# Optimization experiments

Measured on AMD Instinct MI355X. Metric: run time of the kernel, lower is better.

## Reference

```python
import jax, jax.numpy as jnp
import numpy as np

N_NODES = 50000
N_EDGES = 800000
IN_CH = 128
HID = 64
HEADS = 4
OUT_CH = 64
NEG_SLOPE = 0.2


def _add_self_loops(ei, n):
    loops = jnp.tile(jnp.arange(n, dtype=ei.dtype)[None, :], (2, 1))
    return jnp.concatenate([ei, loops], axis=1)


def _gat_conv(x, ei, W, a_s, a_d, b, concat):
    """PyG-style GATConv. x:[N,F], ei:[2,E], W:[F,H*C], a_s/a_d:[H,C]."""
    N = x.shape[0]
    H, C = a_s.shape
    h = (x @ W).reshape(N, H, C)                     # [N,H,C]
    src, dst = ei[0], ei[1]
    al_s = (h * a_s[None]).sum(-1)                   # [N,H]
    al_d = (h * a_d[None]).sum(-1)                   # [N,H]
    logits = jax.nn.leaky_relu(al_s[src] + al_d[dst], NEG_SLOPE)  # [E,H]
    # segment softmax over incoming edges of each dst node
    m = jax.ops.segment_max(logits, dst, num_segments=N)
    m = jax.lax.stop_gradient(jnp.where(jnp.isfinite(m), m, 0.0))
    ex = jnp.exp(logits - m[dst])
    denom = jax.ops.segment_sum(ex, dst, num_segments=N)
    alpha = ex / (denom[dst] + 1e-16)                # [E,H]
    out = jax.ops.segment_sum(alpha[:, :, None] * h[src], dst, num_segments=N)  # [N,H,C]
    out = out.reshape(N, H * C) if concat else out.mean(axis=1)
    return out + b


def _hetero_layer(x, edges, self_loop_flags, W, a_s, a_d, b, concat):
    N = x.shape[0]
    out = None
    for r in range(3):
        ei = _add_self_loops(edges[r], N) if self_loop_flags[r] else edges[r]
        o = _gat_conv(x, ei, W[r], a_s[r], a_d[r], b[r], concat)
        out = o if out is None else out + o
    return out


def setup_inputs() -> dict:
    key = jax.random.key(0)
    ks = jax.random.split(key, 16)
    s = 0.05
    return {
        "x": jax.random.normal(ks[0], (N_NODES, IN_CH), jnp.float32),
        "e_blocks": jax.random.randint(ks[1], (2, N_EDGES), 0, N_NODES),
        "e_spatial": jax.random.randint(ks[2], (2, N_EDGES), 0, N_NODES),
        "e_similar": jax.random.randint(ks[3], (2, N_EDGES), 0, N_NODES),
        "W1": jax.random.normal(ks[4], (3, IN_CH, HEADS * HID), jnp.float32) * s,
        "a1s": jax.random.normal(ks[5], (3, HEADS, HID), jnp.float32) * s,
        "a1d": jax.random.normal(ks[6], (3, HEADS, HID), jnp.float32) * s,
        "b1": jax.random.normal(ks[7], (3, HEADS * HID), jnp.float32) * s,
        "W2": jax.random.normal(ks[8], (3, HEADS * HID, HEADS * HID), jnp.float32) * s,
        "a2s": jax.random.normal(ks[9], (3, HEADS, HID), jnp.float32) * s,
        "a2d": jax.random.normal(ks[10], (3, HEADS, HID), jnp.float32) * s,
        "b2": jax.random.normal(ks[11], (3, HID), jnp.float32) * s,
        "Wl": jax.random.normal(ks[12], (HID, OUT_CH), jnp.float32) * s,
        "bl": jax.random.normal(ks[13], (OUT_CH,), jnp.float32) * s,
    }


def reference(x, e_blocks, e_spatial, e_similar, W1, a1s, a1d, b1,
              W2, a2s, a2d, b2, Wl, bl):
    edges = [e_blocks, e_spatial, e_similar]
    self_loops = [False, True, True]  # 'blocks' has add_self_loops=False
    h = _hetero_layer(x, edges, self_loops, W1, a1s, a1d, b1, concat=True)
    h = jax.nn.relu(h)
    h = _hetero_layer(h, edges, self_loops, W2, a2s, a2d, b2, concat=False)
    h = jax.nn.relu(h)
    return h @ Wl + bl
```

## Files before the change

kernel.cpp:

```cpp
#include <hip/hip_runtime.h>
#include <hip/hip_bf16.h>
#include <hip/hip_fp16.h>

#define NN 50000
#define NE 800000
#define FIN 128
#define HCC 256
#define OC 64
#define NSL 0.2f
#define NT3 (3 * NN)

typedef __attribute__((ext_vector_type(8))) short sh8;
typedef __attribute__((ext_vector_type(8))) unsigned short u16x8;
typedef __attribute__((ext_vector_type(16))) float f32x16;

struct __attribute__((aligned(8))) h4 { __half x, y, z, w; };

__device__ __forceinline__ unsigned short bf_rne(float f) {
  unsigned u = __float_as_uint(f);
  u += 0x7FFF + ((u >> 16) & 1);
  return (unsigned short)(u >> 16);
}

__device__ __forceinline__ float hbits2f(unsigned short u) {
  __half_raw hr; hr.x = u;
  return __half2float((__half)hr);
}

__device__ __forceinline__ float edge_w(float lg) {
  lg = (lg > 0.f) ? lg : NSL * lg;
  return __expf(lg);
}

template<int KK>
__global__ __launch_bounds__(256) void k_prep(const float* __restrict__ W,
                                              short* __restrict__ out) {
  int i = blockIdx.x * 256 + threadIdx.x;
  if (i >= 3 * KK * 256) return;
  int r = i / (KK * 256);
  int rem = i - r * KK * 256;
  int k = rem >> 8;
  int n = rem & 255;
  float f = W[i];
  unsigned short hb = bf_rne(f);
  float hf = __uint_as_float(((unsigned)hb) << 16);
  unsigned short lb = bf_rne(f - hf);
  int cb = n >> 7, c = n & 127, ks8 = k >> 3, kj = k & 7;
  size_t base = (size_t)r * 4 * KK * 128;
  size_t oh = base + ((size_t)((cb * 2 + 0) * (KK / 8) + ks8) * 128 + c) * 8 + kj;
  size_t ol = base + ((size_t)((cb * 2 + 1) * (KK / 8) + ks8) * 128 + c) * 8 + kj;
  out[oh] = (short)hb;
  out[ol] = (short)lb;
}

__global__ void k_hist(const int* __restrict__ dst, int* __restrict__ deg, int n) {
  int i = blockIdx.x * blockDim.x + threadIdx.x;
  int st = gridDim.x * blockDim.x;
  for (; i < n; i += st) atomicAdd(&deg[dst[i]], 1);
}

__global__ __launch_bounds__(1024) void k_bsum(const int* __restrict__ deg3,
                                               int* __restrict__ bsum) {
  __shared__ int s[1024];
  int t = threadIdx.x;
  int i = blockIdx.x * 1024 + t;
  s[t] = (i < NT3) ? deg3[i] : 0;
  __syncthreads();
  for (int off = 512; off > 0; off >>= 1) {
    if (t < off) s[t] += s[t + off];
    __syncthreads();
  }
  if (t == 0) bsum[blockIdx.x] = s[0];
}

__global__ __launch_bounds__(256) void k_scan2(const int* __restrict__ bsum,
                                               int* __restrict__ boffs, int nb) {
  __shared__ int s[256];
  int t = threadIdx.x;
  int v = (t < nb) ? bsum[t] : 0;
  s[t] = v;
  __syncthreads();
  for (int off = 1; off < 256; off <<= 1) {
    int x = (t >= off) ? s[t - off] : 0;
    __syncthreads();
    s[t] += x;
    __syncthreads();
  }
  if (t < nb) boffs[t] = s[t] - v;
}

__global__ __launch_bounds__(1024) void k_rowptr(const int* __restrict__ deg3,
                                                 const int* __restrict__ boffs,
                                                 int* __restrict__ rpA,
                                                 int* __restrict__ cursor3) {
  __shared__ int s[1024];
  int t = threadIdx.x;
  int i = blockIdx.x * 1024 + t;
  int d = (i < NT3) ? deg3[i] : 0;
  s[t] = d;
  __syncthreads();
  for (int off = 1; off < 1024; off <<= 1) {
    int x = (t >= off) ? s[t - off] : 0;
    __syncthreads();
    s[t] += x;
    __syncthreads();
  }
  if (i < NT3) {
    int excl = boffs[blockIdx.x] + s[t] - d;
    int r = (i < NN) ? 0 : ((i < 2 * NN) ? 1 : 2);
    int n = i - r * NN;
    int val = excl - r * NE;
    rpA[r * (NN + 1) + n] = val;
    cursor3[i] = val;
  }
  if (blockIdx.x == 0 && t < 3) rpA[t * (NN + 1) + NN] = NE;
}

__global__ void k_scatter(const int* __restrict__ srcv, const int* __restrict__ dstv,
                          int* __restrict__ cursor, int* __restrict__ csr_src, int n) {
  int i = blockIdx.x * blockDim.x + threadIdx.x;
  int st = gridDim.x * blockDim.x;
  for (; i < n; i += st) {
    int pos = atomicAdd(&cursor[dstv[i]], 1);
    csr_src[pos] = srcv[i];
  }
}

template<int KK, bool AF32>
__global__ __launch_bounds__(256) void k_mgemm(const void* __restrict__ Av,
                                               const short* __restrict__ BcAll,
                                               const float* __restrict__ asfAll,
                                               const float* __restrict__ adfAll,
                                               __half* __restrict__ houtAll,
                                               float* __restrict__ alsAll,
                                               float* __restrict__ aldAll, int M) {
  const int rel = blockIdx.y;
  const short* Bc = BcAll + (size_t)rel * 4 * KK * 128;
  const float* asf = asfAll + rel * HCC;
  const float* adf = adfAll + rel * HCC;
  __half* hout = houtAll + (size_t)rel * NN * HCC;
  float* als = alsAll + (size_t)rel * NN * 4;
  float* ald = aldAll + (size_t)rel * NN * 4;

  const int tid = threadIdx.x;
  const int lane = tid & 63;
  const int w = tid >> 6;
  const int l31 = lane & 31;
  const int lg = lane >> 5;
  const int wrow = blockIdx.x * 64 + (w & 1) * 32;
  const int ch = w >> 1;

  f32x16 acc[4];
#pragma unroll
  for (int t = 0; t < 4; ++t) acc[t] = (f32x16)(0.f);

  const int r = wrow + l31;
  const bool aok = r < M;
  const float* apf = (const float*)Av + (size_t)r * KK;
  const __half* aph = (const __half*)Av + (size_t)r * KK;
  const short* bh = Bc + (size_t)(ch * 2 + 0) * KK * 128 + l31 * 8;
  const short* bl = Bc + (size_t)(ch * 2 + 1) * KK * 128 + l31 * 8;

#pragma unroll 2
  for (int kst = 0; kst < KK / 16; ++kst) {
    const int k0 = kst * 16 + lg * 8;
    float fa[8];
    if (AF32) {
      float4 x0 = make_float4(0.f, 0.f, 0.f, 0.f), x1 = x0;
      if (aok) {
        x0 = *(const float4*)(apf + k0);
        x1 = *(const float4*)(apf + k0 + 4);
      }
      fa[0] = x0.x; fa[1] = x0.y; fa[2] = x0.z; fa[3] = x0.w;
      fa[4] = x1.x; fa[5] = x1.y; fa[6] = x1.z; fa[7] = x1.w;
    } else {
      u16x8 hv = {0, 0, 0, 0, 0, 0, 0, 0};
      if (aok) hv = *(const u16x8*)(aph + k0);
#pragma unroll
      for (int j = 0; j < 8; ++j) fa[j] = hbits2f(hv[j]);
    }
    const int ks8 = kst * 2 + lg;
    const short* bhp = bh + (size_t)ks8 * 1024;
    const short* blp = bl + (size_t)ks8 * 1024;
    sh8 bhf[4], blf[4];
#pragma unroll
    for (int t = 0; t < 4; ++t) {
      bhf[t] = *(const sh8*)(bhp + t * 256);
      blf[t] = *(const sh8*)(blp + t * 256);
    }
    sh8 ahi, alo;
#pragma unroll
    for (int j = 0; j < 8; ++j) {
      float f = fa[j];
      unsigned short hb = bf_rne(f);
      float hf = __uint_as_float(((unsigned)hb) << 16);
      unsigned short lb = bf_rne(f - hf);
      ahi[j] = (short)hb;
      alo[j] = (short)lb;
    }
#pragma unroll
    for (int t = 0; t < 4; ++t) {
      acc[t] = __builtin_amdgcn_mfma_f32_32x32x16_bf16(ahi, bhf[t], acc[t], 0, 0, 0);
      acc[t] = __builtin_amdgcn_mfma_f32_32x32x16_bf16(alo, bhf[t], acc[t], 0, 0, 0);
      acc[t] = __builtin_amdgcn_mfma_f32_32x32x16_bf16(ahi, blf[t], acc[t], 0, 0, 0);
    }
  }

  float asr[4], adr[4];
#pragma unroll
  for (int t = 0; t < 4; ++t) {
    int col = ch * 128 + t * 32 + l31;
    asr[t] = asf[col];
    adr[t] = adf[col];
  }
#pragma unroll
  for (int v = 0; v < 16; ++v) {
    const int rl = (v & 3) + 8 * (v >> 2) + 4 * lg;
    const int row = wrow + rl;
    const bool rok = row < M;
    float s0 = 0.f, s1 = 0.f, d0 = 0.f, d1 = 0.f;
    __half* hp = hout + (size_t)row * 256 + ch * 128 + l31;
#pragma unroll
    for (int t = 0; t < 4; ++t) {
      float dv = acc[t][v];
      if (rok) hp[t * 32] = __float2half(dv);
      if (t < 2) { s0 += dv * asr[t]; d0 += dv * adr[t]; }
      else       { s1 += dv * asr[t]; d1 += dv * adr[t]; }
    }
#pragma unroll
    for (int m = 1; m < 32; m <<= 1) {
      s0 += __shfl_xor(s0, m);
      s1 += __shfl_xor(s1, m);
      d0 += __shfl_xor(d0, m);
      d1 += __shfl_xor(d1, m);
    }
    if (rok && l31 == 0) {
      *(float2*)(als + (size_t)row * 4 + ch * 2) = make_float2(s0, s1);
      *(float2*)(ald + (size_t)row * 4 + ch * 2) = make_float2(d0, d1);
    }
  }
}

template<bool SL>
__device__ __forceinline__ void gat_rel(int n, int head, size_t loff,
                                        const __half* __restrict__ h,
                                        const float* __restrict__ als,
                                        const float* __restrict__ ald,
                                        const int* __restrict__ rp,
                                        const int* __restrict__ cs,
                                        float& ox, float& oy, float& oz, float& ow) {
  float ad = ald[n * 4 + head];
  int rs = rp[n], re = rp[n + 1];
  float ax = 0.f, ay = 0.f, az = 0.f, aw = 0.f, wsum = 0.f;
  int i = rs;
  for (; i + 4 <= re; i += 4) {
    int s0 = cs[i], s1 = cs[i + 1], s2 = cs[i + 2], s3 = cs[i + 3];
    float al0 = als[s0 * 4 + head];
    float al1 = als[s1 * 4 + head];
    float al2 = als[s2 * 4 + head];
    float al3 = als[s3 * 4 + head];
    h4 v0 = *(const h4*)&h[(size_t)s0 * HCC + loff];
    h4 v1 = *(const h4*)&h[(size_t)s1 * HCC + loff];
    h4 v2 = *(const h4*)&h[(size_t)s2 * HCC + loff];
    h4 v3 = *(const h4*)&h[(size_t)s3 * HCC + loff];
    float w0 = edge_w(al0 + ad), w1 = edge_w(al1 + ad);
    float w2 = edge_w(al2 + ad), w3 = edge_w(al3 + ad);
    wsum += (w0 + w1) + (w2 + w3);
    ax = fmaf(w0, __half2float(v0.x), ax); ay = fmaf(w0, __half2float(v0.y), ay);
    az = fmaf(w0, __half2float(v0.z), az); aw = fmaf(w0, __half2float(v0.w), aw);
    ax = fmaf(w1, __half2float(v1.x), ax); ay = fmaf(w1, __half2float(v1.y), ay);
    az = fmaf(w1, __half2float(v1.z), az); aw = fmaf(w1, __half2float(v1.w), aw);
    ax = fmaf(w2, __half2float(v2.x), ax); ay = fmaf(w2, __half2float(v2.y), ay);
    az = fmaf(w2, __half2float(v2.z), az); aw = fmaf(w2, __half2float(v2.w), aw);
    ax = fmaf(w3, __half2float(v3.x), ax); ay = fmaf(w3, __half2float(v3.y), ay);
    az = fmaf(w3, __half2float(v3.z), az); aw = fmaf(w3, __half2float(v3.w), aw);
  }
  for (; i < re; ++i) {
    int s = cs[i];
    float w = edge_w(als[s * 4 + head] + ad);
    wsum += w;
    h4 hv = *(const h4*)&h[(size_t)s * HCC + loff];
    ax = fmaf(w, __half2float(hv.x), ax);
    ay = fmaf(w, __half2float(hv.y), ay);
    az = fmaf(w, __half2float(hv.z), az);
    aw = fmaf(w, __half2float(hv.w), aw);
  }
  if (SL) {
    float w = edge_w(als[n * 4 + head] + ad);
    wsum += w;
    h4 hv = *(const h4*)&h[(size_t)n * HCC + loff];
    ax = fmaf(w, __half2float(hv.x), ax);
    ay = fmaf(w, __half2float(hv.y), ay);
    az = fmaf(w, __half2float(hv.z), az);
    aw = fmaf(w, __half2float(hv.w), aw);
  }
  float inv = 1.0f / (wsum + 1e-16f);
  ox = fmaf(ax, inv, ox);
  oy = fmaf(ay, inv, oy);
  oz = fmaf(az, inv, oz);
  ow = fmaf(aw, inv, ow);
}

template<bool CONCAT>
__global__ __launch_bounds__(256) void k_gather3(const __half* __restrict__ h3,
                                                 const float* __restrict__ als3,
                                                 const float* __restrict__ ald3,
                                                 const int* __restrict__ rpA,
                                                 const int* __restrict__ cs0,
                                                 const int* __restrict__ cs1,
                                                 const int* __restrict__ cs2,
                                                 const float* __restrict__ bias,
                                                 __half* __restrict__ o16,
                                                 float* __restrict__ o32) {
  int gid = blockIdx.x * blockDim.x + threadIdx.x;
  int n = gid >> 6;
  int lane = threadIdx.x & 63;
  if (n >= NN) return;
  int head = lane >> 4;
  size_t loff = (size_t)lane * 4;
  const size_t HS = (size_t)NN * HCC;
  const size_t AS = (size_t)NN * 4;
  float ox = 0.f, oy = 0.f, oz = 0.f, ow = 0.f;
  gat_rel<false>(n, head, loff, h3,          als3,          ald3,          rpA,               cs0, ox, oy, oz, ow);
  gat_rel<true >(n, head, loff, h3 + HS,     als3 + AS,     ald3 + AS,     rpA + (NN + 1),    cs1, ox, oy, oz, ow);
  gat_rel<true >(n, head, loff, h3 + 2 * HS, als3 + 2 * AS, ald3 + 2 * AS, rpA + 2 * (NN + 1), cs2, ox, oy, oz, ow);
  if (CONCAT) {
    float4 b0 = *(const float4*)&bias[lane * 4];
    float4 b1 = *(const float4*)&bias[HCC + lane * 4];
    float4 b2 = *(const float4*)&bias[2 * HCC + lane * 4];
    h4 o;
    o.x = __float2half(fmaxf(ox + b0.x + b1.x + b2.x, 0.f));
    o.y = __float2half(fmaxf(oy + b0.y + b1.y + b2.y, 0.f));
    o.z = __float2half(fmaxf(oz + b0.z + b1.z + b2.z, 0.f));
    o.w = __float2half(fmaxf(ow + b0.w + b1.w + b2.w, 0.f));
    *(h4*)&o16[(size_t)n * HCC + loff] = o;
  } else {
    ox += __shfl_xor(ox, 16); oy += __shfl_xor(oy, 16);
    oz += __shfl_xor(oz, 16); ow += __shfl_xor(ow, 16);
    ox += __shfl_xor(ox, 32); oy += __shfl_xor(oy, 32);
    oz += __shfl_xor(oz, 32); ow += __shfl_xor(ow, 32);
    if (lane < 16) {
      float4 b0 = *(const float4*)&bias[lane * 4];
      float4 b1 = *(const float4*)&bias[OC + lane * 4];
      float4 b2 = *(const float4*)&bias[2 * OC + lane * 4];
      float4 o;
      o.x = 0.25f * ox + b0.x + b1.x + b2.x;
      o.y = 0.25f * oy + b0.y + b1.y + b2.y;
      o.z = 0.25f * oz + b0.z + b1.z + b2.z;
      o.w = 0.25f * ow + b0.w + b1.w + b2.w;
      *(float4*)&o32[(size_t)n * OC + lane * 4] = o;
    }
  }
}

__global__ __launch_bounds__(256) void k_final(const float* __restrict__ out2,
                                               const float* __restrict__ Wl,
                                               const float* __restrict__ bl,
                                               float* __restrict__ outp) {
  __shared__ float Ws[64 * 64];
  __shared__ float bs[64];
  int tid = threadIdx.x;
  for (int i = tid; i < 4096; i += 256) Ws[i] = Wl[i];
  if (tid < 64) bs[tid] = bl[tid];
  __syncthreads();
  int r = blockIdx.x * 4 + (tid >> 6);
  int c = tid & 63;
  if (r >= NN) return;
  const float* xr = &out2[(size_t)r * OC];
  float acc = bs[c];
#pragma unroll
  for (int k = 0; k < 64; ++k) {
    float xv = xr[k];
    xv = (xv > 0.f) ? xv : 0.f;
    acc = fmaf(xv, Ws[k * 64 + c], acc);
  }
  outp[(size_t)r * OC + c] = acc;
}

extern "C" void kernel_launch(void* const* d_in, const int* in_sizes, int n_in,
                              void* d_out, int out_size, void* d_ws, size_t ws_size,
                              hipStream_t stream) {
  const float* x   = (const float*)d_in[0];
  const int* e_b   = (const int*)d_in[1];
  const int* e_sp  = (const int*)d_in[2];
  const int* e_si  = (const int*)d_in[3];
  const float* W1  = (const float*)d_in[4];
  const float* a1s = (const float*)d_in[5];
  const float* a1d = (const float*)d_in[6];
  const float* b1  = (const float*)d_in[7];
  const float* W2  = (const float*)d_in[8];
  const float* a2s = (const float*)d_in[9];
  const float* a2d = (const float*)d_in[10];
  const float* b2  = (const float*)d_in[11];
  const float* Wl  = (const float*)d_in[12];
  const float* bl  = (const float*)d_in[13];
  float* out = (float*)d_out;

  char* ws = (char*)d_ws;
  size_t off = 0;
  auto alloc = [&](size_t b) {
    char* p = ws + off;
    off += (b + 255) & ~(size_t)255;
    return p;
  };
  __half* h3   = (__half*)alloc((size_t)3 * NN * HCC * 2);
  __half* out1h = (__half*)alloc((size_t)NN * HCC * 2);
  float* out2 = (float*)out1h;
  float* als3 = (float*)alloc((size_t)3 * NN * 4 * 4);
  float* ald3 = (float*)alloc((size_t)3 * NN * 4 * 4);
  int* deg3   = (int*)alloc((size_t)NT3 * 4);
  int* cursor3= (int*)alloc((size_t)NT3 * 4);
  int* rpA    = (int*)alloc((size_t)3 * (NN + 1) * 4);
  int* bsum   = (int*)alloc(256 * 4);
  int* boffs  = (int*)alloc(256 * 4);
  short* Wc1  = (short*)alloc((size_t)3 * 4 * FIN * 128 * 2);
  short* Wc2  = (short*)alloc((size_t)3 * 4 * HCC * 128 * 2);
  int* cs[3];
  for (int r = 0; r < 3; ++r) cs[r] = (int*)alloc((size_t)NE * 4);

  const int* edges[3] = {e_b, e_sp, e_si};

  k_prep<FIN><<<(3 * FIN * 256 + 255) / 256, 256, 0, stream>>>(W1, Wc1);
  k_prep<HCC><<<(3 * HCC * 256 + 255) / 256, 256, 0, stream>>>(W2, Wc2);

  hipMemsetAsync(deg3, 0, (size_t)NT3 * 4, stream);
  for (int r = 0; r < 3; ++r)
    k_hist<<<1024, 256, 0, stream>>>(edges[r] + NE, deg3 + r * NN, NE);
  const int NB = (NT3 + 1023) / 1024;
  k_bsum<<<NB, 1024, 0, stream>>>(deg3, bsum);
  k_scan2<<<1, 256, 0, stream>>>(bsum, boffs, NB);
  k_rowptr<<<NB, 1024, 0, stream>>>(deg3, boffs, rpA, cursor3);
  for (int r = 0; r < 3; ++r)
    k_scatter<<<1024, 256, 0, stream>>>(edges[r], edges[r] + NE, cursor3 + r * NN, cs[r], NE);

  const int gblocks = (NN + 63) / 64;
  const int ablocks = (NN * 64) / 256;

  k_mgemm<FIN, true><<<dim3(gblocks, 3), 256, 0, stream>>>(
      x, Wc1, a1s, a1d, h3, als3, ald3, NN);
  k_gather3<true><<<ablocks, 256, 0, stream>>>(
      h3, als3, ald3, rpA, cs[0], cs[1], cs[2], b1, out1h, nullptr);

  k_mgemm<HCC, false><<<dim3(gblocks, 3), 256, 0, stream>>>(
      out1h, Wc2, a2s, a2d, h3, als3, ald3, NN);
  k_gather3<false><<<ablocks, 256, 0, stream>>>(
      h3, als3, ald3, rpA, cs[0], cs[1], cs[2], b2, nullptr, out2);

  k_final<<<(NN + 3) / 4, 256, 0, stream>>>(out2, Wl, bl, out);
}
```

Baseline: 907.1 us.

## Precompute edge weights, pre-split GEMM inputs to bf16 hi/lo, merge CSR kernels

A new per-node kernel computes the exponentiated edge attention weights once, together with per-node weight sums and self-loop weights, before each aggregation pass. The gather kernel then reads these instead of recomputing exp and the softmax denominator for every one of the 64 lanes, and it now unrolls by 8. The bf16 hi/lo split of the GEMM input moves out of the GEMM inner loop: x is split by a separate kernel, and the layer-1 output is written directly as hi/lo bf16 (replacing fp16). The per-relation histogram and scatter launches are merged into single kernels. The cost is extra memory traffic for the edge weight array (3×NE×4 floats) and for the two-plane activations.

```diff
diff --git a/kernel.cpp b/kernel.cpp
--- a/kernel.cpp
+++ b/kernel.cpp
@@ -11,20 +11,15 @@
 #define NT3 (3 * NN)
 
 typedef __attribute__((ext_vector_type(8))) short sh8;
-typedef __attribute__((ext_vector_type(8))) unsigned short u16x8;
 typedef __attribute__((ext_vector_type(16))) float f32x16;
 
 struct __attribute__((aligned(8))) h4 { __half x, y, z, w; };
+struct __attribute__((aligned(8))) s4 { short x, y, z, w; };
 
 __device__ __forceinline__ unsigned short bf_rne(float f) {
   unsigned u = __float_as_uint(f);
   u += 0x7FFF + ((u >> 16) & 1);
   return (unsigned short)(u >> 16);
-}
-
-__device__ __forceinline__ float hbits2f(unsigned short u) {
-  __half_raw hr; hr.x = u;
-  return __half2float((__half)hr);
 }
 
 __device__ __forceinline__ float edge_w(float lg) {
@@ -53,10 +48,32 @@
   out[ol] = (short)lb;
 }
 
-__global__ void k_hist(const int* __restrict__ dst, int* __restrict__ deg, int n) {
+__global__ __launch_bounds__(256) void k_split(const float* __restrict__ x,
+                                               short* __restrict__ xhi,
+                                               short* __restrict__ xlo) {
+  int i = blockIdx.x * 256 + threadIdx.x;
+  if (i >= NN * FIN / 4) return;
+  float4 v = ((const float4*)x)[i];
+  s4 h, l;
+  float f, hf;
+  f = v.x; h.x = (short)bf_rne(f); hf = __uint_as_float(((unsigned)(unsigned short)h.x) << 16); l.x = (short)bf_rne(f - hf);
+  f = v.y; h.y = (short)bf_rne(f); hf = __uint_as_float(((unsigned)(unsigned short)h.y) << 16); l.y = (short)bf_rne(f - hf);
+  f = v.z; h.z = (short)bf_rne(f); hf = __uint_as_float(((unsigned)(unsigned short)h.z) << 16); l.z = (short)bf_rne(f - hf);
+  f = v.w; h.w = (short)bf_rne(f); hf = __uint_as_float(((unsigned)(unsigned short)h.w) << 16); l.w = (short)bf_rne(f - hf);
+  ((s4*)xhi)[i] = h;
+  ((s4*)xlo)[i] = l;
+}
+
+__global__ void k_hist3(const int* __restrict__ e0, const int* __restrict__ e1,
+                        const int* __restrict__ e2, int* __restrict__ deg3) {
   int i = blockIdx.x * blockDim.x + threadIdx.x;
   int st = gridDim.x * blockDim.x;
-  for (; i < n; i += st) atomicAdd(&deg[dst[i]], 1);
+  for (; i < 3 * NE; i += st) {
+    int rel = i / NE;
+    int j = i - rel * NE;
+    const int* e = (rel == 0) ? e0 : ((rel == 1) ? e1 : e2);
+    atomicAdd(&deg3[rel * NN + e[NE + j]], 1);
+  }
 }
 
 __global__ __launch_bounds__(1024) void k_bsum(const int* __restrict__ deg3,
@@ -116,18 +133,23 @@
   if (blockIdx.x == 0 && t < 3) rpA[t * (NN + 1) + NN] = NE;
 }
 
-__global__ void k_scatter(const int* __restrict__ srcv, const int* __restrict__ dstv,
-                          int* __restrict__ cursor, int* __restrict__ csr_src, int n) {
+__global__ void k_scatter3(const int* __restrict__ e0, const int* __restrict__ e1,
+                           const int* __restrict__ e2, int* __restrict__ cursor3,
+                           int* __restrict__ csAll) {
   int i = blockIdx.x * blockDim.x + threadIdx.x;
   int st = gridDim.x * blockDim.x;
-  for (; i < n; i += st) {
-    int pos = atomicAdd(&cursor[dstv[i]], 1);
-    csr_src[pos] = srcv[i];
-  }
-}
-
-template<int KK, bool AF32>
-__global__ __launch_bounds__(256) void k_mgemm(const void* __restrict__ Av,
+  for (; i < 3 * NE; i += st) {
+    int rel = i / NE;
+    int j = i - rel * NE;
+    const int* e = (rel == 0) ? e0 : ((rel == 1) ? e1 : e2);
+    int pos = atomicAdd(&cursor3[rel * NN + e[NE + j]], 1);
+    csAll[(size_t)rel * NE + pos] = e[j];
+  }
+}
+
+template<int KK>
+__global__ __launch_bounds__(256) void k_mgemm(const short* __restrict__ Ahi,
+                                               const short* __restrict__ Alo,
                                                const short* __restrict__ BcAll,
                                                const float* __restrict__ asfAll,
                                                const float* __restrict__ adfAll,
@@ -156,28 +178,18 @@
 
   const int r = wrow + l31;
   const bool aok = r < M;
-  const float* apf = (const float*)Av + (size_t)r * KK;
-  const __half* aph = (const __half*)Av + (size_t)r * KK;
+  const short* ahp = Ahi + (size_t)r * KK;
+  const short* alp = Alo + (size_t)r * KK;
   const short* bh = Bc + (size_t)(ch * 2 + 0) * KK * 128 + l31 * 8;
   const short* bl = Bc + (size_t)(ch * 2 + 1) * KK * 128 + l31 * 8;
 
 #pragma unroll 2
   for (int kst = 0; kst < KK / 16; ++kst) {
     const int k0 = kst * 16 + lg * 8;
-    float fa[8];
-    if (AF32) {
-      float4 x0 = make_float4(0.f, 0.f, 0.f, 0.f), x1 = x0;
-      if (aok) {
-        x0 = *(const float4*)(apf + k0);
-        x1 = *(const float4*)(apf + k0 + 4);
-      }
-      fa[0] = x0.x; fa[1] = x0.y; fa[2] = x0.z; fa[3] = x0.w;
-      fa[4] = x1.x; fa[5] = x1.y; fa[6] = x1.z; fa[7] = x1.w;
-    } else {
-      u16x8 hv = {0, 0, 0, 0, 0, 0, 0, 0};
-      if (aok) hv = *(const u16x8*)(aph + k0);
-#pragma unroll
-      for (int j = 0; j < 8; ++j) fa[j] = hbits2f(hv[j]);
+    sh8 ahi = {0, 0, 0, 0, 0, 0, 0, 0}, alo = ahi;
+    if (aok) {
+      ahi = *(const sh8*)(ahp + k0);
+      alo = *(const sh8*)(alp + k0);
     }
     const int ks8 = kst * 2 + lg;
     const short* bhp = bh + (size_t)ks8 * 1024;
@@ -187,16 +199,6 @@
     for (int t = 0; t < 4; ++t) {
       bhf[t] = *(const sh8*)(bhp + t * 256);
       blf[t] = *(const sh8*)(blp + t * 256);
-    }
-    sh8 ahi, alo;
-#pragma unroll
-    for (int j = 0; j < 8; ++j) {
-      float f = fa[j];
-      unsigned short hb = bf_rne(f);
-      float hf = __uint_as_float(((unsigned)hb) << 16);
-      unsigned short lb = bf_rne(f - hf);
-      ahi[j] = (short)hb;
-      alo[j] = (short)lb;
     }
 #pragma unroll
     for (int t = 0; t < 4; ++t) {
@@ -241,44 +243,83 @@
   }
 }
 
+__global__ __launch_bounds__(256) void k_ew3(const float* __restrict__ als3,
+                                             const float* __restrict__ ald3,
+                                             const int* __restrict__ rpA,
+                                             const int* __restrict__ csAll,
+                                             float* __restrict__ ew3,
+                                             float* __restrict__ wsum3,
+                                             float* __restrict__ ewself3) {
+  int wid = (blockIdx.x * 256 + threadIdx.x) >> 6;
+  int lane = threadIdx.x & 63;
+  if (wid >= NT3) return;
+  int rel = wid / NN;
+  int n = wid - rel * NN;
+  const int* cs = csAll + (size_t)rel * NE;
+  const float* als = als3 + (size_t)rel * NN * 4;
+  const float* ald = ald3 + (size_t)rel * NN * 4;
+  float* ew = ew3 + (size_t)rel * NE * 4;
+  int rs = rpA[rel * (NN + 1) + n];
+  int re = rpA[rel * (NN + 1) + n + 1];
+  int head = lane & 3;
+  int el = lane >> 2;
+  float ad = ald[n * 4 + head];
+  float ws = 0.f;
+  for (int base = rs; base < re; base += 16) {
+    int e = base + el;
+    float w = 0.f;
+    if (e < re) {
+      int s = cs[e];
+      w = edge_w(als[s * 4 + head] + ad);
+      ew[(size_t)e * 4 + head] = w;
+    }
+    ws += w;
+  }
+  ws += __shfl_xor(ws, 4);
+  ws += __shfl_xor(ws, 8);
+  ws += __shfl_xor(ws, 16);
+  ws += __shfl_xor(ws, 32);
+  float wself = 0.f;
+  if (rel > 0) wself = edge_w(als[n * 4 + head] + ad);
+  if (lane < 4) {
+    ewself3[((size_t)rel * NN + n) * 4 + head] = wself;
+    wsum3[((size_t)rel * NN + n) * 4 + head] = ws + wself;
+  }
+}
+
 template<bool SL>
 __device__ __forceinline__ void gat_rel(int n, int head, size_t loff,
                                         const __half* __restrict__ h,
-                                        const float* __restrict__ als,
-                                        const float* __restrict__ ald,
+                                        const float* __restrict__ ew,
+                                        const float* __restrict__ wsum,
+                                        const float* __restrict__ ewself,
                                         const int* __restrict__ rp,
                                         const int* __restrict__ cs,
                                         float& ox, float& oy, float& oz, float& ow) {
-  float ad = ald[n * 4 + head];
   int rs = rp[n], re = rp[n + 1];
-  float ax = 0.f, ay = 0.f, az = 0.f, aw = 0.f, wsum = 0.f;
+  float ax = 0.f, ay = 0.f, az = 0.f, aw = 0.f;
   int i = rs;
-  for (; i + 4 <= re; i += 4) {
-    int s0 = cs[i], s1 = cs[i + 1], s2 = cs[i + 2], s3 = cs[i + 3];
-    float al0 = als[s0 * 4 + head];
-    float al1 = als[s1 * 4 + head];
-    float al2 = als[s2 * 4 + head];
-    float al3 = als[s3 * 4 + head];
-    h4 v0 = *(const h4*)&h[(size_t)s0 * HCC + loff];
-    h4 v1 = *(const h4*)&h[(size_t)s1 * HCC + loff];
-    h4 v2 = *(const h4*)&h[(size_t)s2 * HCC + loff];
-    h4 v3 = *(const h4*)&h[(size_t)s3 * HCC + loff];
-    float w0 = edge_w(al0 + ad), w1 = edge_w(al1 + ad);
-    float w2 = edge_w(al2 + ad), w3 = edge_w(al3 + ad);
-    wsum += (w0 + w1) + (w2 + w3);
-    ax = fmaf(w0, __half2float(v0.x), ax); ay = fmaf(w0, __half2float(v0.y), ay);
-    az = fmaf(w0, __half2float(v0.z), az); aw = fmaf(w0, __half2float(v0.w), aw);
-    ax = fmaf(w1, __half2float(v1.x), ax); ay = fmaf(w1, __half2float(v1.y), ay);
-    az = fmaf(w1, __half2float(v1.z), az); aw = fmaf(w1, __half2float(v1.w), aw);
-    ax = fmaf(w2, __half2float(v2.x), ax); ay = fmaf(w2, __half2float(v2.y), ay);
-    az = fmaf(w2, __half2float(v2.z), az); aw = fmaf(w2, __half2float(v2.w), aw);
-    ax = fmaf(w3, __half2float(v3.x), ax); ay = fmaf(w3, __half2float(v3.y), ay);
-    az = fmaf(w3, __half2float(v3.z), az); aw = fmaf(w3, __half2float(v3.w), aw);
+  for (; i + 8 <= re; i += 8) {
+    int s[8];
+#pragma unroll
+    for (int j = 0; j < 8; ++j) s[j] = cs[i + j];
+    float w[8];
+#pragma unroll
+    for (int j = 0; j < 8; ++j) w[j] = ew[(size_t)(i + j) * 4 + head];
+    h4 v[8];
+#pragma unroll
+    for (int j = 0; j < 8; ++j) v[j] = *(const h4*)&h[(size_t)s[j] * HCC + loff];
+#pragma unroll
+    for (int j = 0; j < 8; ++j) {
+      ax = fmaf(w[j], __half2float(v[j].x), ax);
+      ay = fmaf(w[j], __half2float(v[j].y), ay);
+      az = fmaf(w[j], __half2float(v[j].z), az);
+      aw = fmaf(w[j], __half2float(v[j].w), aw);
+    }
   }
   for (; i < re; ++i) {
     int s = cs[i];
-    float w = edge_w(als[s * 4 + head] + ad);
-    wsum += w;
+    float w = ew[(size_t)i * 4 + head];
     h4 hv = *(const h4*)&h[(size_t)s * HCC + loff];
     ax = fmaf(w, __half2float(hv.x), ax);
     ay = fmaf(w, __half2float(hv.y), ay);
@@ -286,15 +327,14 @@
     aw = fmaf(w, __half2float(hv.w), aw);
   }
   if (SL) {
-    float w = edge_w(als[n * 4 + head] + ad);
-    wsum += w;
+    float w = ewself[n * 4 + head];
     h4 hv = *(const h4*)&h[(size_t)n * HCC + loff];
     ax = fmaf(w, __half2float(hv.x), ax);
     ay = fmaf(w, __half2float(hv.y), ay);
     az = fmaf(w, __half2float(hv.z), az);
     aw = fmaf(w, __half2float(hv.w), aw);
   }
-  float inv = 1.0f / (wsum + 1e-16f);
+  float inv = 1.0f / (wsum[n * 4 + head] + 1e-16f);
   ox = fmaf(ax, inv, ox);
   oy = fmaf(ay, inv, oy);
   oz = fmaf(az, inv, oz);
@@ -303,14 +343,14 @@
 
 template<bool CONCAT>
 __global__ __launch_bounds__(256) void k_gather3(const __half* __restrict__ h3,
-                                                 const float* __restrict__ als3,
-                                                 const float* __restrict__ ald3,
+                                                 const float* __restrict__ ew3,
+                                                 const float* __restrict__ wsum3,
+                                                 const float* __restrict__ ewself3,
                                                  const int* __restrict__ rpA,
-                                                 const int* __restrict__ cs0,
-                                                 const int* __restrict__ cs1,
-                                                 const int* __restrict__ cs2,
+                                                 const int* __restrict__ csAll,
                                                  const float* __restrict__ bias,
-                                                 __half* __restrict__ o16,
+                                                 short* __restrict__ o1hi,
+                                                 short* __restrict__ o1lo,
                                                  float* __restrict__ o32) {
   int gid = blockIdx.x * blockDim.x + threadIdx.x;
   int n = gid >> 6;
@@ -320,20 +360,32 @@
   size_t loff = (size_t)lane * 4;
   const size_t HS = (size_t)NN * HCC;
   const size_t AS = (size_t)NN * 4;
+  const size_t ES = (size_t)NE * 4;
   float ox = 0.f, oy = 0.f, oz = 0.f, ow = 0.f;
-  gat_rel<false>(n, head, loff, h3,          als3,          ald3,          rpA,               cs0, ox, oy, oz, ow);
-  gat_rel<true >(n, head, loff, h3 + HS,     als3 + AS,     ald3 + AS,     rpA + (NN + 1),    cs1, ox, oy, oz, ow);
-  gat_rel<true >(n, head, loff, h3 + 2 * HS, als3 + 2 * AS, ald3 + 2 * AS, rpA + 2 * (NN + 1), cs2, ox, oy, oz, ow);
+  gat_rel<false>(n, head, loff, h3,          ew3,          wsum3,          ewself3,          rpA,                csAll,          ox, oy, oz, ow);
+  gat_rel<true >(n, head, loff, h3 + HS,     ew3 + ES,     wsum3 + AS,     ewself3 + AS,     rpA + (NN + 1),     csAll + NE,     ox, oy, oz, ow);
+  gat_rel<true >(n, head, loff, h3 + 2 * HS, ew3 + 2 * ES, wsum3 + 2 * AS, ewself3 + 2 * AS, rpA + 2 * (NN + 1), csAll + 2 * NE, ox, oy, oz, ow);
   if (CONCAT) {
     float4 b0 = *(const float4*)&bias[lane * 4];
     float4 b1 = *(const float4*)&bias[HCC + lane * 4];
     float4 b2 = *(const float4*)&bias[2 * HCC + lane * 4];
-    h4 o;
-    o.x = __float2half(fmaxf(ox + b0.x + b1.x + b2.x, 0.f));
-    o.y = __float2half(fmaxf(oy + b0.y + b1.y + b2.y, 0.f));
-    o.z = __float2half(fmaxf(oz + b0.z + b1.z + b2.z, 0.f));
-    o.w = __float2half(fmaxf(ow + b0.w + b1.w + b2.w, 0.f));
-    *(h4*)&o16[(size_t)n * HCC + loff] = o;
+    float vv[4];
+    vv[0] = fmaxf(ox + b0.x + b1.x + b2.x, 0.f);
+    vv[1] = fmaxf(oy + b0.y + b1.y + b2.y, 0.f);
+    vv[2] = fmaxf(oz + b0.z + b1.z + b2.z, 0.f);
+    vv[3] = fmaxf(ow + b0.w + b1.w + b2.w, 0.f);
+    s4 hv, lv;
+    short* hp = (short*)&hv;
+    short* lp = (short*)&lv;
+#pragma unroll
+    for (int j = 0; j < 4; ++j) {
+      unsigned short hb = bf_rne(vv[j]);
+      float hf = __uint_as_float(((unsigned)hb) << 16);
+      hp[j] = (short)hb;
+      lp[j] = (short)bf_rne(vv[j] - hf);
+    }
+    *(s4*)&o1hi[(size_t)n * HCC + loff] = hv;
+    *(s4*)&o1lo[(size_t)n * HCC + loff] = lv;
   } else {
     ox += __shfl_xor(ox, 16); oy += __shfl_xor(oy, 16);
     oz += __shfl_xor(oz, 16); ow += __shfl_xor(ow, 16);
@@ -403,48 +455,54 @@
     off += (b + 255) & ~(size_t)255;
     return p;
   };
-  __half* h3   = (__half*)alloc((size_t)3 * NN * HCC * 2);
-  __half* out1h = (__half*)alloc((size_t)NN * HCC * 2);
-  float* out2 = (float*)out1h;
+  __half* h3  = (__half*)alloc((size_t)3 * NN * HCC * 2);
+  short* o1hi = (short*)alloc((size_t)NN * HCC * 2);
+  short* o1lo = (short*)alloc((size_t)NN * HCC * 2);
+  float* out2 = (float*)o1hi;
+  char* U = alloc((size_t)3 * NE * 4 * 4);
+  short* xhi = (short*)U;
+  short* xlo = (short*)(U + (size_t)NN * FIN * 2);
+  float* ew3 = (float*)U;
   float* als3 = (float*)alloc((size_t)3 * NN * 4 * 4);
   float* ald3 = (float*)alloc((size_t)3 * NN * 4 * 4);
-  int* deg3   = (int*)alloc((size_t)NT3 * 4);
-  int* cursor3= (int*)alloc((size_t)NT3 * 4);
-  int* rpA    = (int*)alloc((size_t)3 * (NN + 1) * 4);
-  int* bsum   = (int*)alloc(256 * 4);
-  int* boffs  = (int*)alloc(256 * 4);
-  short* Wc1  = (short*)alloc((size_t)3 * 4 * FIN * 128 * 2);
-  short* Wc2  = (short*)alloc((size_t)3 * 4 * HCC * 128 * 2);
-  int* cs[3];
-  for (int r = 0; r < 3; ++r) cs[r] = (int*)alloc((size_t)NE * 4);
-
-  const int* edges[3] = {e_b, e_sp, e_si};
+  float* wsum3 = (float*)alloc((size_t)3 * NN * 4 * 4);
+  float* ewself3 = (float*)alloc((size_t)3 * NN * 4 * 4);
+  int* deg3    = (int*)alloc((size_t)NT3 * 4);
+  int* cursor3 = (int*)alloc((size_t)NT3 * 4);
+  int* rpA     = (int*)alloc((size_t)3 * (NN + 1) * 4);
+  int* bsum    = (int*)alloc(256 * 4);
+  int* boffs   = (int*)alloc(256 * 4);
+  short* Wc1   = (short*)alloc((size_t)3 * 4 * FIN * 128 * 2);
+  short* Wc2   = (short*)alloc((size_t)3 * 4 * HCC * 128 * 2);
+  int* csAll   = (int*)alloc((size_t)3 * NE * 4);
 
   k_prep<FIN><<<(3 * FIN * 256 + 255) / 256, 256, 0, stream>>>(W1, Wc1);
   k_prep<HCC><<<(3 * HCC * 256 + 255) / 256, 256, 0, stream>>>(W2, Wc2);
+  k_split<<<(NN * FIN / 4 + 255) / 256, 256, 0, stream>>>(x, xhi, xlo);
 
   hipMemsetAsync(deg3, 0, (size_t)NT3 * 4, stream);
-  for (int r = 0; r < 3; ++r)
-    k_hist<<<1024, 256, 0, stream>>>(edges[r] + NE, deg3 + r * NN, NE);
+  k_hist3<<<2048, 256, 0, stream>>>(e_b, e_sp, e_si, deg3);
   const int NB = (NT3 + 1023) / 1024;
   k_bsum<<<NB, 1024, 0, stream>>>(deg3, bsum);
   k_scan2<<<1, 256, 0, stream>>>(bsum, boffs, NB);
   k_rowptr<<<NB, 1024, 0, stream>>>(deg3, boffs, rpA, cursor3);
-  for (int r = 0; r < 3; ++r)
-    k_scatter<<<1024, 256, 0, stream>>>(edges[r], edges[r] + NE, cursor3 + r * NN, cs[r], NE);
+  k_scatter3<<<2048, 256, 0, stream>>>(e_b, e_sp, e_si, cursor3, csAll);
 
   const int gblocks = (NN + 63) / 64;
   const int ablocks = (NN * 64) / 256;
-
-  k_mgemm<FIN, true><<<dim3(gblocks, 3), 256, 0, stream>>>(
-      x, Wc1, a1s, a1d, h3, als3, ald3, NN);
+  const int eblocks = (NT3 + 3) / 4;
+
+  k_mgemm<FIN><<<dim3(gblocks, 3), 256, 0, stream>>>(
+      xhi, xlo, Wc1, a1s, a1d, h3, als3, ald3, NN);
+  k_ew3<<<eblocks, 256, 0, stream>>>(als3, ald3, rpA, csAll, ew3, wsum3, ewself3);
   k_gather3<true><<<ablocks, 256, 0, stream>>>(
-      h3, als3, ald3, rpA, cs[0], cs[1], cs[2], b1, out1h, nullptr);
-
-  k_mgemm<HCC, false><<<dim3(gblocks, 3), 256, 0, stream>>>(
-      out1h, Wc2, a2s, a2d, h3, als3, ald3, NN);
+      h3, ew3, wsum3, ewself3, rpA, csAll, b1, o1hi, o1lo, nullptr);
+
+  k_mgemm<HCC><<<dim3(gblocks, 3), 256, 0, stream>>>(
+      o1hi, o1lo, Wc2, a2s, a2d, h3, als3, ald3, NN);
+  k_ew3<<<eblocks, 256, 0, stream>>>(als3, ald3, rpA, csAll, ew3, wsum3, ewself3);
   k_gather3<false><<<ablocks, 256, 0, stream>>>(
-      h3, als3, ald3, rpA, cs[0], cs[1], cs[2], b2, nullptr, out2);
+      h3, ew3, wsum3, ewself3, rpA, csAll, b2, nullptr, nullptr, out2);
 
   k_final<<<(NN + 3) / 4, 256, 0, stream>>>(out2, Wl, bl, out);
 }
```

After: 1.008 ms. 11.2% more time.
